# Kernel tuning notes

Hardware: AMD Instinct MI355X
Metric: run time of the kernel (lower is better)

Reference implementation:

```python
import jax, jax.numpy as jnp
import numpy as np

# Poincare ball, curvature c = 1.0 (manifold.c)
C = 1.0
SQC = 1.0  # sqrt(C)
EPS = 1e-15
BALL_EPS = 1e-5
ALPHA = 0.1  # params[0]


def _project(x):
    # clip points back inside the open ball
    norm = jnp.linalg.norm(x, axis=-1, keepdims=True)
    maxnorm = (1.0 - BALL_EPS) / SQC
    return jnp.where(norm > maxnorm, x / jnp.maximum(norm, EPS) * maxnorm, x)


def _artanh(x):
    return jnp.arctanh(jnp.clip(x, -1.0 + 1e-7, 1.0 - 1e-7))


def _lambda_x(x):
    # conformal factor lambda_x = 2 / (1 - c||x||^2)
    return 2.0 / jnp.maximum(1.0 - C * jnp.sum(x * x, axis=-1, keepdims=True), EPS)


def _mobius_scalar_mul(r, x):
    n = jnp.maximum(jnp.linalg.norm(x, axis=-1, keepdims=True), EPS)
    return jnp.tanh(r * _artanh(SQC * n)) * x / (SQC * n)


def _mobius_add(x, y):
    x2 = jnp.sum(x * x, axis=-1, keepdims=True)
    y2 = jnp.sum(y * y, axis=-1, keepdims=True)
    xy = jnp.sum(x * y, axis=-1, keepdims=True)
    num = (1.0 + 2.0 * C * xy + C * y2) * x + (1.0 - C * x2) * y
    den = 1.0 + 2.0 * C * xy + C * C * x2 * y2
    return num / jnp.maximum(den, EPS)


def _expmap0(u):
    n = jnp.maximum(jnp.linalg.norm(u, axis=-1, keepdims=True), EPS)
    return jnp.tanh(SQC * n) * u / (SQC * n)


def _mobius_matvec(W, x):
    # Mobius matrix-vector multiply: expmap0-style rescale of x @ W^T
    xn = jnp.maximum(jnp.linalg.norm(x, axis=-1, keepdims=True), EPS)
    mx = x @ W.T
    mxn = jnp.maximum(jnp.linalg.norm(mx, axis=-1, keepdims=True), EPS)
    res = jnp.tanh(mxn / xn * _artanh(SQC * xn)) * mx / (SQC * mxn)
    return _project(res)


def _clamp_abs(x, eps=1e-10):
    return jnp.where(x >= 0, jnp.maximum(x, eps), jnp.minimum(x, -eps))


def weighted_midpoint_spmm(x, src, dst, w, n):
    # gyro-midpoint of neighbors under sparse adjacency weights
    gamma = _lambda_x(x)                                   # [N,1]
    msg = (gamma * x)[src] * w[:, None]                    # [E,d] irregular gather
    num = jax.ops.segment_sum(msg, dst, num_segments=n)    # [N,d]
    den = jax.ops.segment_sum(jnp.abs(w) * (gamma[:, 0] - 1.0)[src], dst,
                              num_segments=n)[:, None]     # [N,1]
    return _project(_mobius_scalar_mul(0.5, num / _clamp_abs(den)))


def weighted_midpoint_pair(a, b, wa, wb):
    # weighted_midpoint(stack([a,b],dim=1), weights=[wa,wb], reducedim=[1])
    ga, gb = _lambda_x(a), _lambda_x(b)
    num = wa * ga * a + wb * gb * b
    den = abs(wa) * (ga - 1.0) + abs(wb) * (gb - 1.0)
    return _project(_mobius_scalar_mul(0.5, num / _clamp_abs(den)))


def setup_inputs() -> dict:
    key = jax.random.key(0)
    kx, kh, kw, kW, kb, ks, kd = jax.random.split(key, 7)
    N, D, E = 100000, 48, 1600000

    def to_ball(u):
        # squash gaussian samples well inside the Poincare ball
        n = jnp.linalg.norm(u, axis=-1, keepdims=True)
        return 0.5 * u / (1.0 + n)

    x = to_ball(jax.random.normal(kx, (N, D), dtype=jnp.float32))
    h_init = to_ball(jax.random.normal(kh, (N, D), dtype=jnp.float32))
    edge_w = jax.random.uniform(kw, (E,), dtype=jnp.float32, minval=0.01, maxval=1.0)
    W = jax.random.normal(kW, (D, D), dtype=jnp.float32) * (1.0 / np.sqrt(D))
    bias = jax.random.normal(kb, (D,), dtype=jnp.float32) * 0.01
    edge_src = jax.random.randint(ks, (E,), 0, N, dtype=jnp.int32)
    edge_dst = jax.random.randint(kd, (E,), 0, N, dtype=jnp.int32)
    return {"x": x, "h_init": h_init, "edge_w": edge_w, "W": W, "bias": bias,
            "edge_src": edge_src, "edge_dst": edge_dst}


def reference(x, h_init, edge_w, W, bias, edge_src, edge_dst):
    n = x.shape[0]
    # 1) sparse adjacency-weighted hyperbolic midpoint aggregation
    support = weighted_midpoint_spmm(x, edge_src, edge_dst, edge_w, n)
    # 2) residual midpoint with h_init, weights [1-alpha, alpha]
    support = weighted_midpoint_pair(support, h_init, 1.0 - ALPHA, ALPHA)
    # 3) Mobius linear (HyperbolicLinearFast, eval-mode dropout, no nonlin)
    h = _mobius_matvec(W, support)
    h = _project(_mobius_add(h, _expmap0(bias[None, :])))
    return h
```

## Files before the change

kernel.cpp:

```cpp
#include <hip/hip_runtime.h>
#include <math.h>

#define D  48
#define DQ 12
#define SPAN 128
#define SHIFT 7
#define PCH  8192
#define PTH  512
#define NPB  16
#define WSTR 52

constexpr float F_EPS   = 1e-15f;
constexpr float MAXNORM = 1.0f - 1e-5f;

__device__ __forceinline__ float artanh_c(float x) {
    x = fminf(x, 1.0f - 1e-7f);
    x = fmaxf(x, -1.0f + 1e-7f);
    return atanhf(x);
}

__device__ __forceinline__ float clampabs(float x) {
    return (x >= 0.0f) ? fmaxf(x, 1e-10f) : fminf(x, -1e-10f);
}

__device__ __forceinline__ unsigned short f2bf(float f) {
    unsigned u = __float_as_uint(f);
    u += 0x7FFFu + ((u >> 16) & 1u);
    return (unsigned short)(u >> 16);
}

__device__ __forceinline__ float bf2f(unsigned short u) {
    return __uint_as_float(((unsigned)u) << 16);
}

__device__ __forceinline__ float fast_tanh(float x) {
    float e = __expf(2.0f * x);
    return 1.0f - __fdividef(2.0f, e + 1.0f);
}
__device__ __forceinline__ float fast_atanh(float x) {
    x = fminf(x, 1.0f - 1e-7f);
    return 0.5f * __logf(__fdividef(1.0f + x, 1.0f - x));
}

__global__ void k_gamma(const float* __restrict__ x, float* __restrict__ gam,
                        int* __restrict__ ghist, int n, int nb)
{
    int i = blockIdx.x * blockDim.x + threadIdx.x;
    if (i < nb) ghist[i] = 0;
    if (i >= n) return;
    const float4* xr = reinterpret_cast<const float4*>(x) + (size_t)i * DQ;
    float s = 0.0f;
#pragma unroll
    for (int q = 0; q < DQ; ++q) {
        float4 v = xr[q];
        s += v.x * v.x + v.y * v.y + v.z * v.z + v.w * v.w;
    }
    gam[i] = 2.0f / fmaxf(1.0f - s, F_EPS);
}

__global__ __launch_bounds__(PTH) void k_hist(const int* __restrict__ dst,
                                              int* __restrict__ ghist, int E, int nb)
{
    __shared__ int h[1024];
    int t = threadIdx.x;
    for (int i = t; i < 1024; i += PTH) h[i] = 0;
    __syncthreads();
    int base = blockIdx.x * PCH;
#pragma unroll 4
    for (int k = 0; k < PCH / PTH; ++k) {
        int i = base + k * PTH + t;
        if (i < E) {
            unsigned b = ((unsigned)dst[i]) >> SHIFT;
            if (b < 1024u) atomicAdd(&h[b], 1);
        }
    }
    __syncthreads();
    for (int i = t; i < nb; i += PTH) {
        int c = h[i];
        if (c) atomicAdd(&ghist[i], c);
    }
}

__global__ __launch_bounds__(1024) void k_scanb(const int* __restrict__ ghist,
                                                int* __restrict__ gstart,
                                                int* __restrict__ gcur, int nb, int E)
{
    __shared__ int sh[1024];
    int t = threadIdx.x;
    int v = (t < nb) ? ghist[t] : 0;
    sh[t] = v;
    __syncthreads();
    for (int off = 1; off < 1024; off <<= 1) {
        int a = sh[t];
        int b = (t >= off) ? sh[t - off] : 0;
        __syncthreads();
        sh[t] = a + b;
        __syncthreads();
    }
    if (t < nb) { int s = sh[t] - v; gstart[t] = s; gcur[t] = s; }
    if (t == 0) gstart[nb] = E;
}

__global__ __launch_bounds__(PTH) void k_part(const int* __restrict__ src,
                                              const int* __restrict__ dst,
                                              const float* __restrict__ w,
                                              const float* __restrict__ gam,
                                              int* __restrict__ gcur,
                                              int2* __restrict__ seg, int E, int nb)
{
    __shared__ int hist[1024];
    __shared__ int base_[1024];
    __shared__ int lcur[1024];
    int t = threadIdx.x;
    for (int i = t; i < 1024; i += PTH) { hist[i] = 0; base_[i] = 0; lcur[i] = 0; }
    __syncthreads();
    int b0 = blockIdx.x * PCH;
#pragma unroll 4
    for (int k = 0; k < PCH / PTH; ++k) {
        int i = b0 + k * PTH + t;
        if (i < E) {
            unsigned b = ((unsigned)dst[i]) >> SHIFT;
            if (b < 1024u) atomicAdd(&hist[b], 1);
        }
    }
    __syncthreads();
    for (int i = t; i < nb; i += PTH) {
        int c = hist[i];
        if (c) base_[i] = atomicAdd(&gcur[i], c);
    }
    __syncthreads();
#pragma unroll 4
    for (int k = 0; k < PCH / PTH; ++k) {
        int i = b0 + k * PTH + t;
        if (i < E) {
            int d = dst[i];
            unsigned b = ((unsigned)d) >> SHIFT;
            if (b < 1024u) {
                int s = src[i];
                float wv = w[i];
                float g  = gam[s];
                unsigned short wb  = f2bf(wv);
                unsigned short wdb = f2bf(fabsf(wv) * (g - 1.0f));
                int pos = base_[b] + atomicAdd(&lcur[b], 1);
                if (pos >= 0 && pos < E) {
                    int2 r;
                    r.x = ((d & (SPAN - 1)) << 24) | (s & 0xFFFFFF);
                    r.y = ((unsigned)wb << 16) | wdb;
                    seg[pos] = r;
                }
            }
        }
    }
}

__global__ __launch_bounds__(256) void k_sortb(
    const int2* __restrict__ seg, const int* __restrict__ gstart,
    int* __restrict__ starts, int2* __restrict__ seg2, int n, int E)
{
    __shared__ int hist[SPAN];
    __shared__ int sb[SPAN];
    __shared__ int cur[SPAN];
    int b = blockIdx.x;
    int t = threadIdx.x;
    if (b == 0 && t == 0) starts[n] = E;
    int segL = gstart[b], segR = gstart[b + 1];
    if (segL < 0) segL = 0;
    if (segR > E) segR = E;
    if (t < SPAN) hist[t] = 0;
    __syncthreads();
    {
        int j = segL + t;
        for (; j + 768 < segR; j += 1024) {
            unsigned d0 = ((unsigned)seg[j      ].x) >> 24;
            unsigned d1 = ((unsigned)seg[j + 256].x) >> 24;
            unsigned d2 = ((unsigned)seg[j + 512].x) >> 24;
            unsigned d3 = ((unsigned)seg[j + 768].x) >> 24;
            atomicAdd(&hist[d0], 1);
            atomicAdd(&hist[d1], 1);
            atomicAdd(&hist[d2], 1);
            atomicAdd(&hist[d3], 1);
        }
        for (; j < segR; j += 256) {
            unsigned dl = ((unsigned)seg[j].x) >> 24;
            atomicAdd(&hist[dl], 1);
        }
    }
    __syncthreads();
    if (t < SPAN) sb[t] = hist[t];
    __syncthreads();
    for (int off = 1; off < SPAN; off <<= 1) {
        int a = 0;
        if (t < SPAN) { a = sb[t]; if (t >= off) a += sb[t - off]; }
        __syncthreads();
        if (t < SPAN) sb[t] = a;
        __syncthreads();
    }
    if (t < SPAN) {
        int ls = sb[t] - hist[t];
        cur[t] = segL + ls;
        int node = b * SPAN + t;
        if (node < n) starts[node] = segL + ls;
    }
    __syncthreads();
    {
        int j = segL + t;
        for (; j + 768 < segR; j += 1024) {
            int2 r0 = seg[j      ];
            int2 r1 = seg[j + 256];
            int2 r2 = seg[j + 512];
            int2 r3 = seg[j + 768];
            int p0 = atomicAdd(&cur[((unsigned)r0.x) >> 24], 1);
            int p1 = atomicAdd(&cur[((unsigned)r1.x) >> 24], 1);
            int p2 = atomicAdd(&cur[((unsigned)r2.x) >> 24], 1);
            int p3 = atomicAdd(&cur[((unsigned)r3.x) >> 24], 1);
            if (p0 >= 0 && p0 < E) seg2[p0] = make_int2(r0.x & 0xFFFFFF, r0.y);
            if (p1 >= 0 && p1 < E) seg2[p1] = make_int2(r1.x & 0xFFFFFF, r1.y);
            if (p2 >= 0 && p2 < E) seg2[p2] = make_int2(r2.x & 0xFFFFFF, r2.y);
            if (p3 >= 0 && p3 < E) seg2[p3] = make_int2(r3.x & 0xFFFFFF, r3.y);
        }
        for (; j < segR; j += 256) {
            int2 r = seg[j];
            int pos = atomicAdd(&cur[((unsigned)r.x) >> 24], 1);
            if (pos >= 0 && pos < E) seg2[pos] = make_int2(r.x & 0xFFFFFF, r.y);
        }
    }
}

__global__ __launch_bounds__(256) void k_prep(const float* __restrict__ x,
                                              const float* __restrict__ gam,
                                              ushort4* __restrict__ ybf, int n)
{
    long long t = (long long)blockIdx.x * blockDim.x + threadIdx.x;
    int node = (int)(t / DQ);
    if (node >= n) return;
    int part = (int)(t % DQ);
    float g = gam[node];
    float4 v = reinterpret_cast<const float4*>(x)[(size_t)node * DQ + part];
    ushort4 o;
    o.x = f2bf(v.x * g);
    o.y = f2bf(v.y * g);
    o.z = f2bf(v.z * g);
    o.w = f2bf(v.w * g);
    ybf[(size_t)node * DQ + part] = o;
}

__global__ __launch_bounds__(256) void k_gather(
    const ushort4* __restrict__ ybf,
    const int* __restrict__ starts,
    const int2* __restrict__ srec,
    float* __restrict__ num, float* __restrict__ den, int n, int E)
{
    long long t = (long long)blockIdx.x * blockDim.x + threadIdx.x;
    int node = (int)(t / DQ);
    if (node >= n) return;
    int part = (int)(t % DQ);
    int j0 = starts[node], j1 = starts[node + 1];
    if (j0 < 0) j0 = 0;
    if (j1 > E) j1 = E;
    float4 acc = make_float4(0.f, 0.f, 0.f, 0.f);
    float dacc = 0.f;
    int j = j0;
    for (; j + 3 < j1; j += 4) {
        int2 r0 = srec[j];
        int2 r1 = srec[j + 1];
        int2 r2 = srec[j + 2];
        int2 r3 = srec[j + 3];
        ushort4 a0 = ybf[(size_t)(r0.x) * DQ + part];
        ushort4 a1 = ybf[(size_t)(r1.x) * DQ + part];
        ushort4 a2 = ybf[(size_t)(r2.x) * DQ + part];
        ushort4 a3 = ybf[(size_t)(r3.x) * DQ + part];
        float w0 = bf2f((unsigned short)(((unsigned)r0.y) >> 16));
        float w1 = bf2f((unsigned short)(((unsigned)r1.y) >> 16));
        float w2 = bf2f((unsigned short)(((unsigned)r2.y) >> 16));
        float w3 = bf2f((unsigned short)(((unsigned)r3.y) >> 16));
        acc.x = fmaf(w0, bf2f(a0.x), acc.x);
        acc.y = fmaf(w0, bf2f(a0.y), acc.y);
        acc.z = fmaf(w0, bf2f(a0.z), acc.z);
        acc.w = fmaf(w0, bf2f(a0.w), acc.w);
        acc.x = fmaf(w1, bf2f(a1.x), acc.x);
        acc.y = fmaf(w1, bf2f(a1.y), acc.y);
        acc.z = fmaf(w1, bf2f(a1.z), acc.z);
        acc.w = fmaf(w1, bf2f(a1.w), acc.w);
        acc.x = fmaf(w2, bf2f(a2.x), acc.x);
        acc.y = fmaf(w2, bf2f(a2.y), acc.y);
        acc.z = fmaf(w2, bf2f(a2.z), acc.z);
        acc.w = fmaf(w2, bf2f(a2.w), acc.w);
        acc.x = fmaf(w3, bf2f(a3.x), acc.x);
        acc.y = fmaf(w3, bf2f(a3.y), acc.y);
        acc.z = fmaf(w3, bf2f(a3.z), acc.z);
        acc.w = fmaf(w3, bf2f(a3.w), acc.w);
        dacc += bf2f((unsigned short)(((unsigned)r0.y) & 0xFFFF))
              + bf2f((unsigned short)(((unsigned)r1.y) & 0xFFFF))
              + bf2f((unsigned short)(((unsigned)r2.y) & 0xFFFF))
              + bf2f((unsigned short)(((unsigned)r3.y) & 0xFFFF));
    }
    for (; j < j1; ++j) {
        int2 r0 = srec[j];
        ushort4 a0 = ybf[(size_t)(r0.x) * DQ + part];
        float w0 = bf2f((unsigned short)(((unsigned)r0.y) >> 16));
        acc.x = fmaf(w0, bf2f(a0.x), acc.x);
        acc.y = fmaf(w0, bf2f(a0.y), acc.y);
        acc.z = fmaf(w0, bf2f(a0.z), acc.z);
        acc.w = fmaf(w0, bf2f(a0.w), acc.w);
        dacc += bf2f((unsigned short)(((unsigned)r0.y) & 0xFFFF));
    }
    reinterpret_cast<float4*>(num)[(size_t)node * DQ + part] = acc;
    if (part == 0) den[node] = dacc;
}

__global__ void k_init_atomic(float* __restrict__ den, float* __restrict__ num, int n)
{
    int i = blockIdx.x * blockDim.x + threadIdx.x;
    if (i >= n) return;
    den[i] = 0.0f;
    float4* nr = reinterpret_cast<float4*>(num) + (size_t)i * DQ;
    float4 z = make_float4(0.f, 0.f, 0.f, 0.f);
#pragma unroll
    for (int q = 0; q < DQ; ++q) nr[q] = z;
}

__global__ void k_edge_atomic(const float* __restrict__ x, const float* __restrict__ gam,
                              const int* __restrict__ src, const int* __restrict__ dst,
                              const float* __restrict__ w,
                              float* __restrict__ num, float* __restrict__ den, int E)
{
    long long t = (long long)blockIdx.x * blockDim.x + threadIdx.x;
    int e = (int)(t / DQ);
    if (e >= E) return;
    int part = (int)(t % DQ);
    int s = src[e];
    int d = dst[e];
    float we = w[e];
    float g  = gam[s];
    float4 xv = reinterpret_cast<const float4*>(x)[(size_t)s * DQ + part];
    float c = we * g;
    float* np_ = num + (size_t)d * D + part * 4;
    atomicAdd(np_ + 0, c * xv.x);
    atomicAdd(np_ + 1, c * xv.y);
    atomicAdd(np_ + 2, c * xv.z);
    atomicAdd(np_ + 3, c * xv.w);
    if (part == 0) atomicAdd(den + d, fabsf(we) * (g - 1.0f));
}

__global__ __launch_bounds__(256) void k_node(
    float* __restrict__ out,
    const float* __restrict__ den,
    const float* __restrict__ h_init,
    const float* __restrict__ Wm,
    const float* __restrict__ bias, int n)
{
    __shared__ float Ws[D * WSTR];
    __shared__ float bs[D];
    __shared__ float aLds[NPB][D];
    int t = threadIdx.x;
    for (int k = t; k < D * D; k += 256) Ws[(k / D) * WSTR + (k % D)] = Wm[k];
    if (t < D) bs[t] = bias[t];
    __syncthreads();

    int grp = t >> 4;
    int lane = t & 15;
    int i = blockIdx.x * NPB + grp;
    bool act = (i < n);

    auto gsum = [](float v) {
        v += __shfl_xor(v, 1, 16);
        v += __shfl_xor(v, 2, 16);
        v += __shfl_xor(v, 4, 16);
        v += __shfl_xor(v, 8, 16);
        return v;
    };

    auto hmp_scale = [](float s) {
        float nrm = sqrtf(s);
        float ncl = fmaxf(nrm, F_EPS);
        float m = fminf(ncl, 1.0f - 1e-7f);
        float sc = __fdividef(__fdividef(m, ncl),
                              1.0f + sqrtf(fmaxf(1.0f - m * m, 0.0f)));
        float rn = nrm * sc;
        if (rn > MAXNORM) sc *= MAXNORM / fmaxf(rn, F_EPS);
        return sc;
    };

    float a0 = 0.f, a1 = 0.f, a2 = 0.f;
    if (act) {
        float dinv = 1.0f / clampabs(den[i]);
        const float* nr = out + (size_t)i * D;
        a0 = nr[lane] * dinv;
        a1 = nr[lane + 16] * dinv;
        a2 = nr[lane + 32] * dinv;
    }
    float s1 = gsum(a0 * a0 + a1 * a1 + a2 * a2);
    float sc1 = hmp_scale(s1);
    a0 *= sc1; a1 *= sc1; a2 *= sc1;
    float sa = s1 * sc1 * sc1;

    float s2, sc2;
    {
        float b0 = 0.f, b1 = 0.f, b2 = 0.f;
        if (act) {
            const float* hr = h_init + (size_t)i * D;
            b0 = hr[lane];
            b1 = hr[lane + 16];
            b2 = hr[lane + 32];
        }
        float sb = gsum(b0 * b0 + b1 * b1 + b2 * b2);
        float ga = 2.0f / fmaxf(1.0f - sa, F_EPS);
        float gb = 2.0f / fmaxf(1.0f - sb, F_EPS);
        const float wa = 0.9f, wb = 0.1f;
        float dinv = 1.0f / clampabs(wa * (ga - 1.0f) + wb * (gb - 1.0f));
        float ca = wa * ga * dinv, cb = wb * gb * dinv;
        a0 = ca * a0 + cb * b0;
        a1 = ca * a1 + cb * b1;
        a2 = ca * a2 + cb * b2;
        s2 = gsum(a0 * a0 + a1 * a1 + a2 * a2);
        sc2 = hmp_scale(s2);
        a0 *= sc2; a1 *= sc2; a2 *= sc2;
    }
    float xn = fmaxf(sqrtf(s2) * sc2, F_EPS);

    aLds[grp][lane]      = a0;
    aLds[grp][lane + 16] = a1;
    aLds[grp][lane + 32] = a2;
    __syncthreads();

    const float4* av4 = reinterpret_cast<const float4*>(aLds[grp]);
    const float4* w04 = reinterpret_cast<const float4*>(&Ws[lane * WSTR]);
    const float4* w14 = reinterpret_cast<const float4*>(&Ws[(lane + 16) * WSTR]);
    const float4* w24 = reinterpret_cast<const float4*>(&Ws[(lane + 32) * WSTR]);
    float acc0 = 0.f, acc1 = 0.f, acc2 = 0.f;
#pragma unroll
    for (int kq = 0; kq < DQ; ++kq) {
        float4 a4 = av4[kq];
        float4 x0 = w04[kq];
        float4 x1 = w14[kq];
        float4 x2 = w24[kq];
        acc0 = fmaf(x0.x, a4.x, acc0); acc0 = fmaf(x0.y, a4.y, acc0);
        acc0 = fmaf(x0.z, a4.z, acc0); acc0 = fmaf(x0.w, a4.w, acc0);
        acc1 = fmaf(x1.x, a4.x, acc1); acc1 = fmaf(x1.y, a4.y, acc1);
        acc1 = fmaf(x1.z, a4.z, acc1); acc1 = fmaf(x1.w, a4.w, acc1);
        acc2 = fmaf(x2.x, a4.x, acc2); acc2 = fmaf(x2.y, a4.y, acc2);
        acc2 = fmaf(x2.z, a4.z, acc2); acc2 = fmaf(x2.w, a4.w, acc2);
    }
    float bl0 = bs[lane], bl1 = bs[lane + 16], bl2 = bs[lane + 32];
    float smx = gsum(acc0 * acc0 + acc1 * acc1 + acc2 * acc2);
    float xyr = gsum(acc0 * bl0 + acc1 * bl1 + acc2 * bl2);
    float bn2 = gsum(bl0 * bl0 + bl1 * bl1 + bl2 * bl2);

    float mxnr = sqrtf(smx);
    float mxn = fmaxf(mxnr, F_EPS);
    float tt = fast_tanh(__fdividef(mxn, xn) * fast_atanh(xn));
    float sc = __fdividef(tt, mxn);
    float rn = mxnr * sc;
    if (rn > MAXNORM) sc *= MAXNORM / fmaxf(rn, F_EPS);

    float bn  = fmaxf(sqrtf(bn2), F_EPS);
    float ebs = __fdividef(fast_tanh(bn), bn);
    float y2  = ebs * ebs * bn2;

    float x2v = sc * sc * smx;
    float xy = sc * ebs * xyr;
    float c1 = 1.0f + 2.0f * xy + y2;
    float c2 = 1.0f - x2v;
    float dn3 = 1.0f / fmaxf(1.0f + 2.0f * xy + x2v * y2, F_EPS);

    float s3 = dn3 * dn3 * (c1 * c1 * sc * sc * smx
                            + 2.0f * c1 * c2 * sc * ebs * xyr
                            + c2 * c2 * ebs * ebs * bn2);
    float nrm3 = sqrtf(s3);
    float fp = (nrm3 > MAXNORM) ? (MAXNORM / fmaxf(nrm3, F_EPS)) : 1.0f;

    float CA = c1 * sc * dn3 * fp;
    float CB = c2 * ebs * dn3 * fp;

    if (act) {
        float* orow = out + (size_t)i * D;
        orow[lane]      = fmaf(CA, acc0, CB * bl0);
        orow[lane + 16] = fmaf(CA, acc1, CB * bl1);
        orow[lane + 32] = fmaf(CA, acc2, CB * bl2);
    }
}

extern "C" void kernel_launch(void* const* d_in, const int* in_sizes, int n_in,
                              void* d_out, int out_size, void* d_ws, size_t ws_size,
                              hipStream_t stream)
{
    const float* x      = (const float*)d_in[0];
    const float* h_init = (const float*)d_in[1];
    const float* edge_w = (const float*)d_in[2];
    const float* W      = (const float*)d_in[3];
    const float* bias   = (const float*)d_in[4];
    const int*   esrc   = (const int*)d_in[5];
    const int*   edst   = (const int*)d_in[6];
    float* out = (float*)d_out;

    int n = in_sizes[0] / D;
    int E = in_sizes[2];
    int nb = (n + SPAN - 1) >> SHIFT;

    char* p = (char*)d_ws;
    float* gam    = (float*)p;             p += (size_t)n * 4;
    float* den    = (float*)p;             p += (size_t)n * 4;
    int*   ghist  = (int*)p;               p += (size_t)nb * 4;
    int*   gstart = (int*)p;               p += (size_t)(nb + 1) * 4;
    int*   gcur   = (int*)p;               p += (size_t)nb * 4;
    int*   starts = (int*)p;               p += (size_t)(n + 1) * 4;
    p = (char*)(((uintptr_t)p + 15) & ~(uintptr_t)15);
    int2*  seg    = (int2*)p;              p += (size_t)E * 8;
    int2*  seg2   = (int2*)p;              p += (size_t)E * 8;
    size_t need1 = (size_t)(p - (char*)d_ws);
    ushort4* ybf = (ushort4*)seg;
    bool ybf_fits = ((size_t)E * 8 >= (size_t)n * D * 2);

    k_gamma<<<(n + 255) / 256, 256, 0, stream>>>(x, gam, ghist, n, nb);

    bool shape_ok = (nb <= 1024) && (n < (1 << 24));
    if (shape_ok && ybf_fits && need1 <= ws_size) {
        int pb = (E + PCH - 1) / PCH;
        k_hist<<<pb, PTH, 0, stream>>>(edst, ghist, E, nb);
        k_scanb<<<1, 1024, 0, stream>>>(ghist, gstart, gcur, nb, E);
        k_part<<<pb, PTH, 0, stream>>>(esrc, edst, edge_w, gam, gcur, seg, E, nb);
        k_sortb<<<nb, 256, 0, stream>>>(seg, gstart, starts, seg2, n, E);
        long long tot = (long long)n * DQ;
        int gg = (int)((tot + 255) / 256);
        k_prep<<<gg, 256, 0, stream>>>(x, gam, ybf, n);
        k_gather<<<gg, 256, 0, stream>>>(ybf, starts, seg2, out, den, n, E);
    } else {
        k_init_atomic<<<(n + 255) / 256, 256, 0, stream>>>(den, out, n);
        long long tot = (long long)E * DQ;
        k_edge_atomic<<<(int)((tot + 255) / 256), 256, 0, stream>>>(x, gam, esrc, edst, edge_w, out, den, E);
    }

    k_node<<<(n + NPB - 1) / NPB, 256, 0, stream>>>(out, den, h_init, W, bias, n);
}
```

Before: 150.1 us.

## Fuse neighbor gather with node-wise Mobius linear and move gamma into node table

The gather kernel is merged with the per-node midpoint/Mobius-linear kernel, so each 16-lane group aggregates one node's neighbors and then runs the residual midpoint, matvec and bias add without writing num/den to global memory. The per-source gamma-1 term is stored as a 13th slot in each bf16 node row, which removes the random gam[src] gather from the partition kernel. Edge weights are now kept as full fp32 in the records. The partition chunk size is also halved. The trade-off is fewer threads per node during the gather (lanes 13-15 idle, one lane does the denominator), a wider node row, and a W-matrix LDS load in every fused block.

```diff
diff --git a/kernel.cpp b/kernel.cpp
--- a/kernel.cpp
+++ b/kernel.cpp
@@ -5,10 +5,11 @@
 #define DQ 12
 #define SPAN 128
 #define SHIFT 7
-#define PCH  8192
+#define PCH  4096
 #define PTH  512
 #define NPB  16
 #define WSTR 52
+#define YROW 13
 
 constexpr float F_EPS   = 1e-15f;
 constexpr float MAXNORM = 1.0f - 1e-5f;
@@ -31,6 +32,10 @@
 
 __device__ __forceinline__ float bf2f(unsigned short u) {
     return __uint_as_float(((unsigned)u) << 16);
+}
+
+__device__ __forceinline__ float gm1f(ushort4 a) {
+    return __uint_as_float((unsigned)a.x | ((unsigned)a.y << 16));
 }
 
 __device__ __forceinline__ float fast_tanh(float x) {
@@ -66,7 +71,7 @@
     for (int i = t; i < 1024; i += PTH) h[i] = 0;
     __syncthreads();
     int base = blockIdx.x * PCH;
-#pragma unroll 4
+#pragma unroll
     for (int k = 0; k < PCH / PTH; ++k) {
         int i = base + k * PTH + t;
         if (i < E) {
@@ -104,7 +109,6 @@
 __global__ __launch_bounds__(PTH) void k_part(const int* __restrict__ src,
                                               const int* __restrict__ dst,
                                               const float* __restrict__ w,
-                                              const float* __restrict__ gam,
                                               int* __restrict__ gcur,
                                               int2* __restrict__ seg, int E, int nb)
 {
@@ -115,7 +119,7 @@
     for (int i = t; i < 1024; i += PTH) { hist[i] = 0; base_[i] = 0; lcur[i] = 0; }
     __syncthreads();
     int b0 = blockIdx.x * PCH;
-#pragma unroll 4
+#pragma unroll
     for (int k = 0; k < PCH / PTH; ++k) {
         int i = b0 + k * PTH + t;
         if (i < E) {
@@ -129,23 +133,18 @@
         if (c) base_[i] = atomicAdd(&gcur[i], c);
     }
     __syncthreads();
-#pragma unroll 4
+#pragma unroll
     for (int k = 0; k < PCH / PTH; ++k) {
         int i = b0 + k * PTH + t;
         if (i < E) {
             int d = dst[i];
             unsigned b = ((unsigned)d) >> SHIFT;
             if (b < 1024u) {
-                int s = src[i];
-                float wv = w[i];
-                float g  = gam[s];
-                unsigned short wb  = f2bf(wv);
-                unsigned short wdb = f2bf(fabsf(wv) * (g - 1.0f));
                 int pos = base_[b] + atomicAdd(&lcur[b], 1);
                 if (pos >= 0 && pos < E) {
                     int2 r;
-                    r.x = ((d & (SPAN - 1)) << 24) | (s & 0xFFFFFF);
-                    r.y = ((unsigned)wb << 16) | wdb;
+                    r.x = ((d & (SPAN - 1)) << 24) | (src[i] & 0xFFFFFF);
+                    r.y = __float_as_int(w[i]);
                     seg[pos] = r;
                 }
             }
@@ -231,32 +230,72 @@
                                               ushort4* __restrict__ ybf, int n)
 {
     long long t = (long long)blockIdx.x * blockDim.x + threadIdx.x;
-    int node = (int)(t / DQ);
+    int node = (int)(t / YROW);
     if (node >= n) return;
-    int part = (int)(t % DQ);
+    int slot = (int)(t % YROW);
     float g = gam[node];
-    float4 v = reinterpret_cast<const float4*>(x)[(size_t)node * DQ + part];
     ushort4 o;
-    o.x = f2bf(v.x * g);
-    o.y = f2bf(v.y * g);
-    o.z = f2bf(v.z * g);
-    o.w = f2bf(v.w * g);
-    ybf[(size_t)node * DQ + part] = o;
-}
-
-__global__ __launch_bounds__(256) void k_gather(
+    if (slot < 12) {
+        float4 v = reinterpret_cast<const float4*>(x)[(size_t)node * DQ + slot];
+        o.x = f2bf(v.x * g);
+        o.y = f2bf(v.y * g);
+        o.z = f2bf(v.z * g);
+        o.w = f2bf(v.w * g);
+    } else {
+        unsigned u = __float_as_uint(g - 1.0f);
+        o.x = (unsigned short)(u & 0xFFFFu);
+        o.y = (unsigned short)(u >> 16);
+        o.z = 0; o.w = 0;
+    }
+    ybf[(size_t)node * YROW + slot] = o;
+}
+
+__global__ __launch_bounds__(256) void k_fuse(
     const ushort4* __restrict__ ybf,
     const int* __restrict__ starts,
     const int2* __restrict__ srec,
-    float* __restrict__ num, float* __restrict__ den, int n, int E)
-{
-    long long t = (long long)blockIdx.x * blockDim.x + threadIdx.x;
-    int node = (int)(t / DQ);
-    if (node >= n) return;
-    int part = (int)(t % DQ);
-    int j0 = starts[node], j1 = starts[node + 1];
-    if (j0 < 0) j0 = 0;
-    if (j1 > E) j1 = E;
+    const float* __restrict__ h_init,
+    const float* __restrict__ Wm,
+    const float* __restrict__ bias,
+    float* __restrict__ out, int n, int E)
+{
+    __shared__ float Ws[D * WSTR];
+    __shared__ float bs[D];
+    __shared__ float aLds[NPB][WSTR];
+    int t = threadIdx.x;
+    for (int k = t; k < D * D; k += 256) Ws[(k / D) * WSTR + (k % D)] = Wm[k];
+    if (t < D) bs[t] = bias[t];
+
+    int grp = t >> 4;
+    int lane = t & 15;
+    int i = blockIdx.x * NPB + grp;
+    bool act = (i < n);
+
+    auto gsum = [](float v) {
+        v += __shfl_xor(v, 1, 16);
+        v += __shfl_xor(v, 2, 16);
+        v += __shfl_xor(v, 4, 16);
+        v += __shfl_xor(v, 8, 16);
+        return v;
+    };
+    auto hmp_scale = [](float s) {
+        float nrm = sqrtf(s);
+        float ncl = fmaxf(nrm, F_EPS);
+        float m = fminf(ncl, 1.0f - 1e-7f);
+        float sc = __fdividef(__fdividef(m, ncl),
+                              1.0f + sqrtf(fmaxf(1.0f - m * m, 0.0f)));
+        float rn = nrm * sc;
+        if (rn > MAXNORM) sc *= MAXNORM / fmaxf(rn, F_EPS);
+        return sc;
+    };
+
+    int j0 = 0, j1 = 0;
+    if (act) {
+        j0 = starts[i]; j1 = starts[i + 1];
+        if (j0 < 0) j0 = 0;
+        if (j1 > E) j1 = E;
+    }
+    int pp = (lane < 12) ? lane : 12;
     float4 acc = make_float4(0.f, 0.f, 0.f, 0.f);
     float dacc = 0.f;
     int j = j0;
@@ -265,47 +304,150 @@
         int2 r1 = srec[j + 1];
         int2 r2 = srec[j + 2];
         int2 r3 = srec[j + 3];
-        ushort4 a0 = ybf[(size_t)(r0.x) * DQ + part];
-        ushort4 a1 = ybf[(size_t)(r1.x) * DQ + part];
-        ushort4 a2 = ybf[(size_t)(r2.x) * DQ + part];
-        ushort4 a3 = ybf[(size_t)(r3.x) * DQ + part];
-        float w0 = bf2f((unsigned short)(((unsigned)r0.y) >> 16));
-        float w1 = bf2f((unsigned short)(((unsigned)r1.y) >> 16));
-        float w2 = bf2f((unsigned short)(((unsigned)r2.y) >> 16));
-        float w3 = bf2f((unsigned short)(((unsigned)r3.y) >> 16));
-        acc.x = fmaf(w0, bf2f(a0.x), acc.x);
-        acc.y = fmaf(w0, bf2f(a0.y), acc.y);
-        acc.z = fmaf(w0, bf2f(a0.z), acc.z);
-        acc.w = fmaf(w0, bf2f(a0.w), acc.w);
-        acc.x = fmaf(w1, bf2f(a1.x), acc.x);
-        acc.y = fmaf(w1, bf2f(a1.y), acc.y);
-        acc.z = fmaf(w1, bf2f(a1.z), acc.z);
-        acc.w = fmaf(w1, bf2f(a1.w), acc.w);
-        acc.x = fmaf(w2, bf2f(a2.x), acc.x);
-        acc.y = fmaf(w2, bf2f(a2.y), acc.y);
-        acc.z = fmaf(w2, bf2f(a2.z), acc.z);
-        acc.w = fmaf(w2, bf2f(a2.w), acc.w);
-        acc.x = fmaf(w3, bf2f(a3.x), acc.x);
-        acc.y = fmaf(w3, bf2f(a3.y), acc.y);
-        acc.z = fmaf(w3, bf2f(a3.z), acc.z);
-        acc.w = fmaf(w3, bf2f(a3.w), acc.w);
-        dacc += bf2f((unsigned short)(((unsigned)r0.y) & 0xFFFF))
-              + bf2f((unsigned short)(((unsigned)r1.y) & 0xFFFF))
-              + bf2f((unsigned short)(((unsigned)r2.y) & 0xFFFF))
-              + bf2f((unsigned short)(((unsigned)r3.y) & 0xFFFF));
+        ushort4 a0 = ybf[(size_t)r0.x * YROW + pp];
+        ushort4 a1 = ybf[(size_t)r1.x * YROW + pp];
+        ushort4 a2 = ybf[(size_t)r2.x * YROW + pp];
+        ushort4 a3 = ybf[(size_t)r3.x * YROW + pp];
+        float w0 = __int_as_float(r0.y);
+        float w1 = __int_as_float(r1.y);
+        float w2 = __int_as_float(r2.y);
+        float w3 = __int_as_float(r3.y);
+        if (lane < 12) {
+            acc.x = fmaf(w0, bf2f(a0.x), acc.x);
+            acc.y = fmaf(w0, bf2f(a0.y), acc.y);
+            acc.z = fmaf(w0, bf2f(a0.z), acc.z);
+            acc.w = fmaf(w0, bf2f(a0.w), acc.w);
+            acc.x = fmaf(w1, bf2f(a1.x), acc.x);
+            acc.y = fmaf(w1, bf2f(a1.y), acc.y);
+            acc.z = fmaf(w1, bf2f(a1.z), acc.z);
+            acc.w = fmaf(w1, bf2f(a1.w), acc.w);
+            acc.x = fmaf(w2, bf2f(a2.x), acc.x);
+            acc.y = fmaf(w2, bf2f(a2.y), acc.y);
+            acc.z = fmaf(w2, bf2f(a2.z), acc.z);
+            acc.w = fmaf(w2, bf2f(a2.w), acc.w);
+            acc.x = fmaf(w3, bf2f(a3.x), acc.x);
+            acc.y = fmaf(w3, bf2f(a3.y), acc.y);
+            acc.z = fmaf(w3, bf2f(a3.z), acc.z);
+            acc.w = fmaf(w3, bf2f(a3.w), acc.w);
+        } else if (lane == 12) {
+            dacc += fabsf(w0) * gm1f(a0) + fabsf(w1) * gm1f(a1)
+                  + fabsf(w2) * gm1f(a2) + fabsf(w3) * gm1f(a3);
+        }
     }
     for (; j < j1; ++j) {
         int2 r0 = srec[j];
-        ushort4 a0 = ybf[(size_t)(r0.x) * DQ + part];
-        float w0 = bf2f((unsigned short)(((unsigned)r0.y) >> 16));
-        acc.x = fmaf(w0, bf2f(a0.x), acc.x);
-        acc.y = fmaf(w0, bf2f(a0.y), acc.y);
-        acc.z = fmaf(w0, bf2f(a0.z), acc.z);
-        acc.w = fmaf(w0, bf2f(a0.w), acc.w);
-        dacc += bf2f((unsigned short)(((unsigned)r0.y) & 0xFFFF));
-    }
-    reinterpret_cast<float4*>(num)[(size_t)node * DQ + part] = acc;
-    if (part == 0) den[node] = dacc;
+        ushort4 a0 = ybf[(size_t)r0.x * YROW + pp];
+        float w0 = __int_as_float(r0.y);
+        if (lane < 12) {
+            acc.x = fmaf(w0, bf2f(a0.x), acc.x);
+            acc.y = fmaf(w0, bf2f(a0.y), acc.y);
+            acc.z = fmaf(w0, bf2f(a0.z), acc.z);
+            acc.w = fmaf(w0, bf2f(a0.w), acc.w);
+        } else if (lane == 12) {
+            dacc += fabsf(w0) * gm1f(a0);
+        }
+    }
+
+    float dv = __shfl(dacc, 12, 16);
+
+    if (lane < 12)
+        reinterpret_cast<float4*>(&aLds[grp][0])[lane] = acc;
+    __syncthreads();
+
+    float dinv = 1.0f / clampabs(dv);
+    float a0 = aLds[grp][lane]      * dinv;
+    float a1 = aLds[grp][lane + 16] * dinv;
+    float a2 = aLds[grp][lane + 32] * dinv;
+
+    float s1 = gsum(a0 * a0 + a1 * a1 + a2 * a2);
+    float sc1 = hmp_scale(s1);
+    a0 *= sc1; a1 *= sc1; a2 *= sc1;
+    float sa = s1 * sc1 * sc1;
+
+    float s2, sc2;
+    {
+        float b0 = 0.f, b1 = 0.f, b2 = 0.f;
+        if (act) {
+            const float* hr = h_init + (size_t)i * D;
+            b0 = hr[lane];
+            b1 = hr[lane + 16];
+            b2 = hr[lane + 32];
+        }
+        float sb = gsum(b0 * b0 + b1 * b1 + b2 * b2);
+        float ga = 2.0f / fmaxf(1.0f - sa, F_EPS);
+        float gb = 2.0f / fmaxf(1.0f - sb, F_EPS);
+        const float wa = 0.9f, wb = 0.1f;
+        float dinv2 = 1.0f / clampabs(wa * (ga - 1.0f) + wb * (gb - 1.0f));
+        float ca = wa * ga * dinv2, cb = wb * gb * dinv2;
+        a0 = ca * a0 + cb * b0;
+        a1 = ca * a1 + cb * b1;
+        a2 = ca * a2 + cb * b2;
+        s2 = gsum(a0 * a0 + a1 * a1 + a2 * a2);
+        sc2 = hmp_scale(s2);
+        a0 *= sc2; a1 *= sc2; a2 *= sc2;
+    }
+    float xn = fmaxf(sqrtf(s2) * sc2, F_EPS);
+
+    aLds[grp][lane]      = a0;
+    aLds[grp][lane + 16] = a1;
+    aLds[grp][lane + 32] = a2;
+    __syncthreads();
+
+    const float4* av4 = reinterpret_cast<const float4*>(&aLds[grp][0]);
+    const float4* w04 = reinterpret_cast<const float4*>(&Ws[lane * WSTR]);
+    const float4* w14 = reinterpret_cast<const float4*>(&Ws[(lane + 16) * WSTR]);
+    const float4* w24 = reinterpret_cast<const float4*>(&Ws[(lane + 32) * WSTR]);
+    float acc0 = 0.f, acc1 = 0.f, acc2 = 0.f;
+#pragma unroll
+    for (int kq = 0; kq < DQ; ++kq) {
+        float4 a4 = av4[kq];
+        float4 x0 = w04[kq];
+        float4 x1 = w14[kq];
+        float4 x2 = w24[kq];
+        acc0 = fmaf(x0.x, a4.x, acc0); acc0 = fmaf(x0.y, a4.y, acc0);
+        acc0 = fmaf(x0.z, a4.z, acc0); acc0 = fmaf(x0.w, a4.w, acc0);
+        acc1 = fmaf(x1.x, a4.x, acc1); acc1 = fmaf(x1.y, a4.y, acc1);
+        acc1 = fmaf(x1.z, a4.z, acc1); acc1 = fmaf(x1.w, a4.w, acc1);
+        acc2 = fmaf(x2.x, a4.x, acc2); acc2 = fmaf(x2.y, a4.y, acc2);
+        acc2 = fmaf(x2.z, a4.z, acc2); acc2 = fmaf(x2.w, a4.w, acc2);
+    }
+    float bl0 = bs[lane], bl1 = bs[lane + 16], bl2 = bs[lane + 32];
+    float smx = gsum(acc0 * acc0 + acc1 * acc1 + acc2 * acc2);
+    float xyr = gsum(acc0 * bl0 + acc1 * bl1 + acc2 * bl2);
+    float bn2 = gsum(bl0 * bl0 + bl1 * bl1 + bl2 * bl2);
+
+    float mxnr = sqrtf(smx);
+    float mxn = fmaxf(mxnr, F_EPS);
+    float tt = fast_tanh(__fdividef(mxn, xn) * fast_atanh(xn));
+    float sc = __fdividef(tt, mxn);
+    float rn = mxnr * sc;
+    if (rn > MAXNORM) sc *= MAXNORM / fmaxf(rn, F_EPS);
+
+    float bn  = fmaxf(sqrtf(bn2), F_EPS);
+    float ebs = __fdividef(fast_tanh(bn), bn);
+    float y2  = ebs * ebs * bn2;
+
+    float x2v = sc * sc * smx;
+    float xy = sc * ebs * xyr;
+    float c1 = 1.0f + 2.0f * xy + y2;
+    float c2 = 1.0f - x2v;
+    float dn3 = 1.0f / fmaxf(1.0f + 2.0f * xy + x2v * y2, F_EPS);
+
+    float s3 = dn3 * dn3 * (c1 * c1 * sc * sc * smx
+                            + 2.0f * c1 * c2 * sc * ebs * xyr
+                            + c2 * c2 * ebs * ebs * bn2);
+    float nrm3 = sqrtf(s3);
+    float fp = (nrm3 > MAXNORM) ? (MAXNORM / fmaxf(nrm3, F_EPS)) : 1.0f;
+
+    float CA = c1 * sc * dn3 * fp;
+    float CB = c2 * ebs * dn3 * fp;
+
+    if (act) {
+        float* orow = out + (size_t)i * D;
+        orow[lane]      = fmaf(CA, acc0, CB * bl0);
+        orow[lane + 16] = fmaf(CA, acc1, CB * bl1);
+        orow[lane + 32] = fmaf(CA, acc2, CB * bl2);
+    }
 }
 
 __global__ void k_init_atomic(float* __restrict__ den, float* __restrict__ num, int n)
@@ -342,7 +484,7 @@
     if (part == 0) atomicAdd(den + d, fabsf(we) * (g - 1.0f));
 }
 
-__global__ __launch_bounds__(256) void k_node(
+__global__ __launch_bounds__(256) void k_node_fb(
     float* __restrict__ out,
     const float* __restrict__ den,
     const float* __restrict__ h_init,
@@ -351,7 +493,7 @@
 {
     __shared__ float Ws[D * WSTR];
     __shared__ float bs[D];
-    __shared__ float aLds[NPB][D];
+    __shared__ float aLds[NPB][WSTR];
     int t = threadIdx.x;
     for (int k = t; k < D * D; k += 256) Ws[(k / D) * WSTR + (k % D)] = Wm[k];
     if (t < D) bs[t] = bias[t];
@@ -369,7 +511,6 @@
         v += __shfl_xor(v, 8, 16);
         return v;
     };
-
     auto hmp_scale = [](float s) {
         float nrm = sqrtf(s);
         float ncl = fmaxf(nrm, F_EPS);
@@ -423,7 +564,7 @@
     aLds[grp][lane + 32] = a2;
     __syncthreads();
 
-    const float4* av4 = reinterpret_cast<const float4*>(aLds[grp]);
+    const float4* av4 = reinterpret_cast<const float4*>(&aLds[grp][0]);
     const float4* w04 = reinterpret_cast<const float4*>(&Ws[lane * WSTR]);
     const float4* w14 = reinterpret_cast<const float4*>(&Ws[(lane + 16) * WSTR]);
     const float4* w24 = reinterpret_cast<const float4*>(&Ws[(lane + 32) * WSTR]);
@@ -509,7 +650,7 @@
     int2*  seg2   = (int2*)p;              p += (size_t)E * 8;
     size_t need1 = (size_t)(p - (char*)d_ws);
     ushort4* ybf = (ushort4*)seg;
-    bool ybf_fits = ((size_t)E * 8 >= (size_t)n * D * 2);
+    bool ybf_fits = ((size_t)E * 8 >= (size_t)n * YROW * 8);
 
     k_gamma<<<(n + 255) / 256, 256, 0, stream>>>(x, gam, ghist, n, nb);
 
@@ -518,17 +659,16 @@
         int pb = (E + PCH - 1) / PCH;
         k_hist<<<pb, PTH, 0, stream>>>(edst, ghist, E, nb);
         k_scanb<<<1, 1024, 0, stream>>>(ghist, gstart, gcur, nb, E);
-        k_part<<<pb, PTH, 0, stream>>>(esrc, edst, edge_w, gam, gcur, seg, E, nb);
+        k_part<<<pb, PTH, 0, stream>>>(esrc, edst, edge_w, gcur, seg, E, nb);
         k_sortb<<<nb, 256, 0, stream>>>(seg, gstart, starts, seg2, n, E);
-        long long tot = (long long)n * DQ;
-        int gg = (int)((tot + 255) / 256);
-        k_prep<<<gg, 256, 0, stream>>>(x, gam, ybf, n);
-        k_gather<<<gg, 256, 0, stream>>>(ybf, starts, seg2, out, den, n, E);
+        long long pt = (long long)n * YROW;
+        k_prep<<<(int)((pt + 255) / 256), 256, 0, stream>>>(x, gam, ybf, n);
+        k_fuse<<<(n + NPB - 1) / NPB, 256, 0, stream>>>(
+            ybf, starts, seg2, h_init, W, bias, out, n, E);
     } else {
         k_init_atomic<<<(n + 255) / 256, 256, 0, stream>>>(den, out, n);
         long long tot = (long long)E * DQ;
         k_edge_atomic<<<(int)((tot + 255) / 256), 256, 0, stream>>>(x, gam, esrc, edst, edge_w, out, den, E);
-    }
-
-    k_node<<<(n + NPB - 1) / NPB, 256, 0, stream>>>(out, den, h_init, W, bias, n);
-}
+        k_node_fb<<<(n + NPB - 1) / NPB, 256, 0, stream>>>(out, den, h_init, W, bias, n);
+    }
+}
```

Result: faster. 144.7 us (-3.6%).
